# Kernel optimization log

Hardware: AMD Instinct MI355X
Metric: run time of the kernel (lower is better)

## Reference

```python
import jax, jax.numpy as jnp
import numpy as np

B, C, N, F = 256, 4, 64, 256   # batch, in_channels, neighbors, in_features
OC, OF = 8, 256                # out_channels, out_features


def setup_inputs() -> dict:
    key = jax.random.key(0)
    k1, k2, k3, k4, k5 = jax.random.split(key, 5)
    x = jax.random.normal(k1, (B, C, F), dtype=jnp.float32)
    neighbor = jax.random.normal(k2, (B, N, C, F), dtype=jnp.float32)
    # torch.nn.Linear weights are (out_features, in_features)
    W_att1 = jax.random.normal(k3, (C, F), dtype=jnp.float32) / np.sqrt(F).astype(np.float32)
    W_att2 = jax.random.normal(k4, (C, F), dtype=jnp.float32) / np.sqrt(F).astype(np.float32)
    # Conv1d weight: (out_c*out_f, 2C, F); kernel_size==F makes it a dense contraction
    W_conv = jax.random.normal(k5, (OC * OF, 2 * C, F), dtype=jnp.float32) / np.sqrt(2 * C * F).astype(np.float32)
    return {"x": x, "neighbor": neighbor, "W_att1": W_att1, "W_att2": W_att2, "W_conv": W_conv}


def reference(x, neighbor, W_att1, W_att2, W_conv):
    # --- attention weights: einsum 'ci,nkl->n' = sum(att1(x_i)) * sum_{k,l} att2(y_i)[n]
    s1 = jnp.sum(x @ W_att1.T, axis=(1, 2))              # (B,)
    s2 = jnp.sum(neighbor @ W_att2.T, axis=(2, 3))       # (B, N)
    w = jax.nn.softmax(s1[:, None] * s2, axis=1)         # softmax over neighbors (dim 0 per-sample)

    # --- feature adjacency: einsum 'ca,ncb,n->cab' vectorized over batch
    fadj = jnp.einsum('bcx,bncy,bn->bcxy', x, neighbor, w)   # (B, C, F, F)
    fadj = fadj + jnp.swapaxes(fadj, -1, -2)
    # sgnroot
    fadj = jnp.sign(fadj) * jnp.sqrt(jnp.clip(jnp.abs(fadj), 1e-8, None))
    # row normalize over dim -2, NaN -> 0
    adj = fadj / (jnp.abs(fadj).sum(axis=-2, keepdims=True) + 1e-7)
    adj = jnp.where(jnp.isnan(adj), jnp.float32(0.0), adj)

    # --- transform: cat([adj @ x, x], channel) then full-width conv1d (dense contraction)
    h = jnp.einsum('bcxy,bcy->bcx', adj, x)              # (B, C, F)
    z = jnp.concatenate([h, x], axis=1)                  # (B, 2C, F)
    out = jnp.einsum('bcf,ocf->bo', z, W_conv).reshape(B, OC, OF)
    return out, adj
```

## Files before the change

### kernel.cpp

```cpp
#include <hip/hip_runtime.h>
#include <hip/hip_bf16.h>
#include <math.h>


typedef __bf16 bf16x8 __attribute__((ext_vector_type(8)));
typedef __bf16 bf16x4 __attribute__((ext_vector_type(4)));
typedef float f32x4 __attribute__((ext_vector_type(4)));

#define NB 256
#define NC 4
#define NN 64
#define NF 256
#define NO 2048

__global__ __launch_bounds__(256) void k_scores(
    const float* __restrict__ x, const float* __restrict__ nb,
    const float* __restrict__ W1, const float* __restrict__ W2,
    float* __restrict__ s1, float* __restrict__ s2)
{
  __shared__ float red[4];
  int t = threadIdx.x;
  int gid = blockIdx.x;
  float val;
  if (gid < NB * NN) {
    float w = W2[t] + W2[256 + t] + W2[512 + t] + W2[768 + t];
    const float* p = nb + (size_t)gid * 1024;
    val = w * (p[t] + p[256 + t] + p[512 + t] + p[768 + t]);
  } else {
    int b = gid - NB * NN;
    float w = W1[t] + W1[256 + t] + W1[512 + t] + W1[768 + t];
    const float* p = x + (size_t)b * 1024;
    val = w * (p[t] + p[256 + t] + p[512 + t] + p[768 + t]);
  }
  for (int off = 32; off > 0; off >>= 1) val += __shfl_down(val, off);
  int wid = t >> 6;
  if ((t & 63) == 0) red[wid] = val;
  __syncthreads();
  if (t == 0) {
    float s = red[0] + red[1] + red[2] + red[3];
    if (gid < NB * NN) s2[gid] = s;
    else s1[gid - NB * NN] = s;
  }
}

__global__ __launch_bounds__(256) void k_cvt(
    const float* __restrict__ Wc, const float* __restrict__ x,
    __hip_bfloat16* __restrict__ Wcb, __hip_bfloat16* __restrict__ zbf)
{
  int idx = blockIdx.x * 256 + threadIdx.x;
  if (idx < 1048576) {
    float4 v = ((const float4*)Wc)[idx];
    bf16x4 o = { (__bf16)v.x, (__bf16)v.y, (__bf16)v.z, (__bf16)v.w };
    ((bf16x4*)Wcb)[idx] = o;
  } else {
    int i = idx - 1048576;
    int e = i * 4;
    int b = e >> 10, r = e & 1023;
    float4 v = ((const float4*)x)[i];
    bf16x4 o = { (__bf16)v.x, (__bf16)v.y, (__bf16)v.z, (__bf16)v.w };
    *(bf16x4*)(zbf + (size_t)b * 2048 + 1024 + r) = o;
  }
}

__global__ __launch_bounds__(256) void k_adj(
    const float* __restrict__ x, const float* __restrict__ nb,
    const float* __restrict__ s1, const float* __restrict__ s2,
    float* __restrict__ adj, float* __restrict__ hf,
    __hip_bfloat16* __restrict__ zbf)
{
  __shared__ float xs[256], ns[256], invs[256], wsh[64];
  __shared__ float part[4][256];
  int t = threadIdx.x;
  int w = t >> 6, l = t & 63;
  int blk = blockIdx.x;
  int b = blk >> 2, c = blk & 3;

  if (t < 64) {
    float v = s1[b] * s2[b * 64 + t];
    float m = v;
    for (int off = 32; off > 0; off >>= 1) m = fmaxf(m, __shfl_xor(m, off));
    float e = expf(v - m);
    float s = e;
    for (int off = 32; off > 0; off >>= 1) s += __shfl_xor(s, off);
    wsh[t] = e / s;
  }
  __syncthreads();

  float acc = 0.f;
  const float* pb = nb + (size_t)b * 65536 + c * 256 + t;
  #pragma unroll 8
  for (int n = 0; n < 64; ++n) acc = fmaf(wsh[n], pb[(size_t)n * 1024], acc);
  ns[t] = acc;
  xs[t] = x[(size_t)blk * 256 + t];
  __syncthreads();

  int j0 = l * 4;
  float4 xv = *(const float4*)&xs[j0];
  float4 nv = *(const float4*)&ns[j0];
  int i0 = w * 64;

  float4 cs = {0.f, 0.f, 0.f, 0.f};
  #pragma unroll 4
  for (int ii = 0; ii < 64; ++ii) {
    int i = i0 + ii;
    float xi = xs[i], ni = ns[i];
    float v0 = fmaf(xi, nv.x, xv.x * ni);
    float v1 = fmaf(xi, nv.y, xv.y * ni);
    float v2 = fmaf(xi, nv.z, xv.z * ni);
    float v3 = fmaf(xi, nv.w, xv.w * ni);
    float r0 = __builtin_amdgcn_sqrtf(fmaxf(fabsf(v0), 1e-8f));
    float r1 = __builtin_amdgcn_sqrtf(fmaxf(fabsf(v1), 1e-8f));
    float r2 = __builtin_amdgcn_sqrtf(fmaxf(fabsf(v2), 1e-8f));
    float r3 = __builtin_amdgcn_sqrtf(fmaxf(fabsf(v3), 1e-8f));
    cs.x += (v0 != 0.f) ? r0 : 0.f;
    cs.y += (v1 != 0.f) ? r1 : 0.f;
    cs.z += (v2 != 0.f) ? r2 : 0.f;
    cs.w += (v3 != 0.f) ? r3 : 0.f;
  }
  *(float4*)&part[w][j0] = cs;
  __syncthreads();
  invs[t] = 1.f / (part[0][t] + part[1][t] + part[2][t] + part[3][t] + 1e-7f);
  __syncthreads();

  float4 iv = *(const float4*)&invs[j0];
  float4 ha = {0.f, 0.f, 0.f, 0.f};
  float* ab = adj + (size_t)blk * 65536;
  #pragma unroll 4
  for (int ii = 0; ii < 64; ++ii) {
    int i = i0 + ii;
    float xi = xs[i], ni = ns[i];
    float pix = invs[i] * xi;
    float v0 = fmaf(xi, nv.x, xv.x * ni);
    float v1 = fmaf(xi, nv.y, xv.y * ni);
    float v2 = fmaf(xi, nv.z, xv.z * ni);
    float v3 = fmaf(xi, nv.w, xv.w * ni);
    float g0 = (v0 != 0.f) ? copysignf(__builtin_amdgcn_sqrtf(fmaxf(fabsf(v0), 1e-8f)), v0) : 0.f;
    float g1 = (v1 != 0.f) ? copysignf(__builtin_amdgcn_sqrtf(fmaxf(fabsf(v1), 1e-8f)), v1) : 0.f;
    float g2 = (v2 != 0.f) ? copysignf(__builtin_amdgcn_sqrtf(fmaxf(fabsf(v2), 1e-8f)), v2) : 0.f;
    float g3 = (v3 != 0.f) ? copysignf(__builtin_amdgcn_sqrtf(fmaxf(fabsf(v3), 1e-8f)), v3) : 0.f;
    f32x4 o = { g0 * iv.x, g1 * iv.y, g2 * iv.z, g3 * iv.w };
    __builtin_nontemporal_store(o, (f32x4*)&ab[(size_t)i * 256 + j0]);
    ha.x = fmaf(g0, pix, ha.x);
    ha.y = fmaf(g1, pix, ha.y);
    ha.z = fmaf(g2, pix, ha.z);
    ha.w = fmaf(g3, pix, ha.w);
  }
  __syncthreads();
  *(float4*)&part[w][j0] = ha;
  __syncthreads();
  float hsum = part[0][t] + part[1][t] + part[2][t] + part[3][t];
  if (zbf) zbf[(size_t)b * 2048 + c * 256 + t] = __float2bfloat16(hsum);
  else     hf[(size_t)blk * 256 + t] = hsum;
}

__global__ __launch_bounds__(256) void k_gemm(
    const __hip_bfloat16* __restrict__ zb, const __hip_bfloat16* __restrict__ Wcb,
    float* __restrict__ out)
{
  int tid = threadIdx.x;
  int wave = tid >> 6, lane = tid & 63;
  int g = lane >> 4, r = lane & 15;
  int bm = blockIdx.x & 7, bn = blockIdx.x >> 3;
  int m0 = bm * 32 + (wave & 1) * 16;
  int n0 = bn * 32 + (wave >> 1) * 16;

  const bf16x8* pa = (const bf16x8*)(zb  + (size_t)(m0 + r) * 2048 + g * 8);
  const bf16x8* pw = (const bf16x8*)(Wcb + (size_t)(n0 + r) * 2048 + g * 8);

  f32x4 acc0 = {0.f, 0.f, 0.f, 0.f}, acc1 = {0.f, 0.f, 0.f, 0.f};
  #pragma unroll 4
  for (int ks = 0; ks < 64; ks += 2) {
    bf16x8 a0 = pa[ks * 4];
    bf16x8 b0 = pw[ks * 4];
    bf16x8 a1 = pa[ks * 4 + 4];
    bf16x8 b1 = pw[ks * 4 + 4];
    acc0 = __builtin_amdgcn_mfma_f32_16x16x32_bf16(a0, b0, acc0, 0, 0, 0);
    acc1 = __builtin_amdgcn_mfma_f32_16x16x32_bf16(a1, b1, acc1, 0, 0, 0);
  }
  acc0 += acc1;
  #pragma unroll
  for (int q = 0; q < 4; ++q) {
    int row = m0 + g * 4 + q;
    __builtin_nontemporal_store(acc0[q], &out[(size_t)row * 2048 + n0 + r]);
  }
}

__device__ inline bf16x8 cvt8_p(const float* p) {
  const float4* q = reinterpret_cast<const float4*>(p);
  float4 a = q[0], bq = q[1];
  bf16x8 r;
  r[0] = (__bf16)a.x;  r[1] = (__bf16)a.y;  r[2] = (__bf16)a.z;  r[3] = (__bf16)a.w;
  r[4] = (__bf16)bq.x; r[5] = (__bf16)bq.y; r[6] = (__bf16)bq.z; r[7] = (__bf16)bq.w;
  return r;
}

__global__ __launch_bounds__(256) void k_gemm_f32(
    const float* __restrict__ h, const float* __restrict__ x,
    const float* __restrict__ Wc, float* __restrict__ out)
{
  int tid = threadIdx.x;
  int wave = tid >> 6, lane = tid & 63;
  int g = lane >> 4, r = lane & 15;
  int bm = blockIdx.x & 3, bn = blockIdx.x >> 2;
  int m0 = bm * 64 + wave * 16;
  int n0 = bn * 32;
  int arow = m0 + r;
  int koff = g * 8;

  const float* za = h + (size_t)arow * 1024 + koff;
  const float* zb = x + (size_t)arow * 1024 + koff;
  const float* w0 = Wc + (size_t)(n0 + r) * 2048 + koff;
  const float* w1 = Wc + (size_t)(n0 + 16 + r) * 2048 + koff;

  f32x4 acc0 = {0.f, 0.f, 0.f, 0.f}, acc1 = {0.f, 0.f, 0.f, 0.f};
  #pragma unroll 4
  for (int ks = 0; ks < 32; ++ks) {
    bf16x8 a  = cvt8_p(za + ks * 32);
    bf16x8 b0 = cvt8_p(w0 + ks * 32);
    bf16x8 b1 = cvt8_p(w1 + ks * 32);
    acc0 = __builtin_amdgcn_mfma_f32_16x16x32_bf16(a, b0, acc0, 0, 0, 0);
    acc1 = __builtin_amdgcn_mfma_f32_16x16x32_bf16(a, b1, acc1, 0, 0, 0);
  }
  #pragma unroll 4
  for (int ks = 0; ks < 32; ++ks) {
    bf16x8 a  = cvt8_p(zb + ks * 32);
    bf16x8 b0 = cvt8_p(w0 + 1024 + ks * 32);
    bf16x8 b1 = cvt8_p(w1 + 1024 + ks * 32);
    acc0 = __builtin_amdgcn_mfma_f32_16x16x32_bf16(a, b0, acc0, 0, 0, 0);
    acc1 = __builtin_amdgcn_mfma_f32_16x16x32_bf16(a, b1, acc1, 0, 0, 0);
  }
  #pragma unroll
  for (int q = 0; q < 4; ++q) {
    int row = m0 + g * 4 + q;
    out[(size_t)row * 2048 + n0 + r]      = acc0[q];
    out[(size_t)row * 2048 + n0 + 16 + r] = acc1[q];
  }
}

extern "C" void kernel_launch(void* const* d_in, const int* in_sizes, int n_in,
                              void* d_out, int out_size, void* d_ws, size_t ws_size,
                              hipStream_t stream) {
  const float* x  = (const float*)d_in[0];
  const float* nb = (const float*)d_in[1];
  const float* W1 = (const float*)d_in[2];
  const float* W2 = (const float*)d_in[3];
  const float* Wc = (const float*)d_in[4];
  float* out = (float*)d_out;
  float* adj = out + (size_t)NB * NO;

  char* ws = (char*)d_ws;
  const size_t ZBF_B = 1048576;
  const size_t WCB_B = 8388608;
  bool fast = ws_size >= ZBF_B + WCB_B + 66560;

  if (fast) {
    __hip_bfloat16* zbf = (__hip_bfloat16*)ws;
    __hip_bfloat16* Wcb = (__hip_bfloat16*)(ws + ZBF_B);
    float* s1 = (float*)(ws + ZBF_B + WCB_B);
    float* s2 = s1 + 256;
    k_scores<<<NB * NN + NB, 256, 0, stream>>>(x, nb, W1, W2, s1, s2);
    k_cvt<<<4352, 256, 0, stream>>>(Wc, x, Wcb, zbf);
    k_adj<<<NB * NC, 256, 0, stream>>>(x, nb, s1, s2, adj, nullptr, zbf);
    k_gemm<<<512, 256, 0, stream>>>(zbf, Wcb, out);
  } else {
    float* hws = (float*)d_ws;
    float* s1  = hws + 262144;
    float* s2  = s1 + 256;
    k_scores<<<NB * NN + NB, 256, 0, stream>>>(x, nb, W1, W2, s1, s2);
    k_adj<<<NB * NC, 256, 0, stream>>>(x, nb, s1, s2, adj, hws, nullptr);
    k_gemm_f32<<<256, 256, 0, stream>>>(hws, x, Wc, out);
  }
}
```

Measured before the change: 112.4 us.

## Split adjacency store into separate wide kernel and merge scores with conversion

Fuses the score and bf16-conversion kernels into one launch that uses float4 loads for the scores. Moves the heavy 256MB adjacency write out of the per-(b,c) kernel into a separate kernel with 4x more blocks, recomputing the entries from saved ns and inverse-norm vectors. The neighbor-weighted sum now reads float4 across waves with a shared-memory reduction. This adds an extra kernel launch and recomputes the sqrt work, in exchange for better write parallelism on the store-bound adjacency output. The fast path needs a larger workspace, and if that is not available it falls back to the old path.

Result: slower. 137.2 us (+22.1%).

```diff
diff --git a/kernel.cpp b/kernel.cpp
--- a/kernel.cpp
+++ b/kernel.cpp
@@ -13,7 +13,218 @@
 #define NF 256
 #define NO 2048
 
-__global__ __launch_bounds__(256) void k_scores(
+__global__ __launch_bounds__(256) void k_pre(
+    const float* __restrict__ x, const float* __restrict__ nb,
+    const float* __restrict__ W1, const float* __restrict__ W2,
+    const float* __restrict__ Wc,
+    __hip_bfloat16* __restrict__ Wcb, __hip_bfloat16* __restrict__ zbf,
+    float* __restrict__ s1, float* __restrict__ s2)
+{
+  __shared__ float red[4];
+  int t = threadIdx.x;
+  int gid = blockIdx.x;
+
+  if (gid < 16640) {
+    int fi = t & 63;
+    const float4* Wf4 = (const float4*)((gid < 16384) ? W2 : W1);
+    float4 w0 = Wf4[fi], w1 = Wf4[64 + fi], w2 = Wf4[128 + fi], w3 = Wf4[192 + fi];
+    float4 wv = { w0.x + w1.x + w2.x + w3.x,
+                  w0.y + w1.y + w2.y + w3.y,
+                  w0.z + w1.z + w2.z + w3.z,
+                  w0.w + w1.w + w2.w + w3.w };
+    const float4* src = (gid < 16384) ? ((const float4*)nb + (size_t)gid * 256)
+                                      : ((const float4*)x + (size_t)(gid - 16384) * 256);
+    float4 nv = src[t];
+    float val = fmaf(nv.x, wv.x, fmaf(nv.y, wv.y, fmaf(nv.z, wv.z, nv.w * wv.w)));
+    for (int off = 32; off > 0; off >>= 1) val += __shfl_down(val, off);
+    if ((t & 63) == 0) red[t >> 6] = val;
+    __syncthreads();
+    if (t == 0) {
+      float s = red[0] + red[1] + red[2] + red[3];
+      if (gid < 16384) s2[gid] = s;
+      else s1[gid - 16384] = s;
+    }
+  } else if (gid < 20736) {
+    int idx = (gid - 16640) * 256 + t;
+    float4 v = ((const float4*)Wc)[idx];
+    bf16x4 o = { (__bf16)v.x, (__bf16)v.y, (__bf16)v.z, (__bf16)v.w };
+    ((bf16x4*)Wcb)[idx] = o;
+  } else {
+    int i = (gid - 20736) * 256 + t;
+    int e = i * 4;
+    int b = e >> 10, r = e & 1023;
+    float4 v = ((const float4*)x)[i];
+    bf16x4 o = { (__bf16)v.x, (__bf16)v.y, (__bf16)v.z, (__bf16)v.w };
+    *(bf16x4*)(zbf + (size_t)b * 2048 + 1024 + r) = o;
+  }
+}
+
+__global__ __launch_bounds__(256) void k_nw(
+    const float* __restrict__ x, const float* __restrict__ nb,
+    const float* __restrict__ s1, const float* __restrict__ s2,
+    float* __restrict__ nsArr, float* __restrict__ invArr,
+    __hip_bfloat16* __restrict__ zbf)
+{
+  __shared__ float xs[256], ns[256], invs[256], wsh[64];
+  __shared__ float part[4][256];
+  int t = threadIdx.x;
+  int w = t >> 6, l = t & 63;
+  int blk = blockIdx.x;
+  int b = blk >> 2, c = blk & 3;
+
+  if (t < 64) {
+    float v = s1[b] * s2[b * 64 + t];
+    float m = v;
+    for (int off = 32; off > 0; off >>= 1) m = fmaxf(m, __shfl_xor(m, off));
+    float e = expf(v - m);
+    float s = e;
+    for (int off = 32; off > 0; off >>= 1) s += __shfl_xor(s, off);
+    wsh[t] = e / s;
+  }
+  xs[t] = x[(size_t)blk * 256 + t];
+  __syncthreads();
+
+  const float4* nb4 = (const float4*)(nb + (size_t)b * 65536 + c * 256);
+  float4 a4 = {0.f, 0.f, 0.f, 0.f};
+  #pragma unroll
+  for (int k = 0; k < 16; ++k) {
+    int n = w + 4 * k;
+    float4 v = nb4[(size_t)n * 256 + l];
+    float wn = wsh[n];
+    a4.x = fmaf(wn, v.x, a4.x);
+    a4.y = fmaf(wn, v.y, a4.y);
+    a4.z = fmaf(wn, v.z, a4.z);
+    a4.w = fmaf(wn, v.w, a4.w);
+  }
+  *(float4*)&part[w][l * 4] = a4;
+  __syncthreads();
+  ns[t] = part[0][t] + part[1][t] + part[2][t] + part[3][t];
+  __syncthreads();
+
+  int j0 = l * 4;
+  float4 xv = *(const float4*)&xs[j0];
+  float4 nv = *(const float4*)&ns[j0];
+  int i0 = w * 64;
+
+  float4 cs = {0.f, 0.f, 0.f, 0.f};
+  #pragma unroll 4
+  for (int ii = 0; ii < 64; ++ii) {
+    int i = i0 + ii;
+    float xi = xs[i], ni = ns[i];
+    float v0 = fmaf(xi, nv.x, xv.x * ni);
+    float v1 = fmaf(xi, nv.y, xv.y * ni);
+    float v2 = fmaf(xi, nv.z, xv.z * ni);
+    float v3 = fmaf(xi, nv.w, xv.w * ni);
+    cs.x += (v0 != 0.f) ? __builtin_amdgcn_sqrtf(fmaxf(fabsf(v0), 1e-8f)) : 0.f;
+    cs.y += (v1 != 0.f) ? __builtin_amdgcn_sqrtf(fmaxf(fabsf(v1), 1e-8f)) : 0.f;
+    cs.z += (v2 != 0.f) ? __builtin_amdgcn_sqrtf(fmaxf(fabsf(v2), 1e-8f)) : 0.f;
+    cs.w += (v3 != 0.f) ? __builtin_amdgcn_sqrtf(fmaxf(fabsf(v3), 1e-8f)) : 0.f;
+  }
+  *(float4*)&part[w][j0] = cs;
+  __syncthreads();
+  invs[t] = 1.f / (part[0][t] + part[1][t] + part[2][t] + part[3][t] + 1e-7f);
+  nsArr[(size_t)blk * 256 + t] = ns[t];
+  __syncthreads();
+  invArr[(size_t)blk * 256 + t] = invs[t];
+
+  float4 ha = {0.f, 0.f, 0.f, 0.f};
+  #pragma unroll 4
+  for (int ii = 0; ii < 64; ++ii) {
+    int i = i0 + ii;
+    float xi = xs[i], ni = ns[i];
+    float pix = invs[i] * xi;
+    float v0 = fmaf(xi, nv.x, xv.x * ni);
+    float v1 = fmaf(xi, nv.y, xv.y * ni);
+    float v2 = fmaf(xi, nv.z, xv.z * ni);
+    float v3 = fmaf(xi, nv.w, xv.w * ni);
+    float g0 = (v0 != 0.f) ? copysignf(__builtin_amdgcn_sqrtf(fmaxf(fabsf(v0), 1e-8f)), v0) : 0.f;
+    float g1 = (v1 != 0.f) ? copysignf(__builtin_amdgcn_sqrtf(fmaxf(fabsf(v1), 1e-8f)), v1) : 0.f;
+    float g2 = (v2 != 0.f) ? copysignf(__builtin_amdgcn_sqrtf(fmaxf(fabsf(v2), 1e-8f)), v2) : 0.f;
+    float g3 = (v3 != 0.f) ? copysignf(__builtin_amdgcn_sqrtf(fmaxf(fabsf(v3), 1e-8f)), v3) : 0.f;
+    ha.x = fmaf(g0, pix, ha.x);
+    ha.y = fmaf(g1, pix, ha.y);
+    ha.z = fmaf(g2, pix, ha.z);
+    ha.w = fmaf(g3, pix, ha.w);
+  }
+  __syncthreads();
+  *(float4*)&part[w][j0] = ha;
+  __syncthreads();
+  float hsum = part[0][t] + part[1][t] + part[2][t] + part[3][t];
+  zbf[(size_t)b * 2048 + c * 256 + t] = __float2bfloat16(hsum);
+}
+
+__global__ __launch_bounds__(256) void k_adj_store(
+    const float* __restrict__ x, const float* __restrict__ nsArr,
+    const float* __restrict__ invArr, float* __restrict__ adj)
+{
+  __shared__ float xs[256], ns[256], invs[256];
+  int t = threadIdx.x;
+  int w = t >> 6, l = t & 63;
+  int blk = blockIdx.x;
+  int bc = blk >> 2, q = blk & 3;
+
+  xs[t]   = x[(size_t)bc * 256 + t];
+  ns[t]   = nsArr[(size_t)bc * 256 + t];
+  invs[t] = invArr[(size_t)bc * 256 + t];
+  __syncthreads();
+
+  int j0 = l * 4;
+  float4 xv = *(const float4*)&xs[j0];
+  float4 nv = *(const float4*)&ns[j0];
+  float4 iv = *(const float4*)&invs[j0];
+  float* ab = adj + (size_t)bc * 65536;
+  int i0 = q * 64 + w * 16;
+
+  #pragma unroll 4
+  for (int ii = 0; ii < 16; ++ii) {
+    int i = i0 + ii;
+    float xi = xs[i], ni = ns[i];
+    float v0 = fmaf(xi, nv.x, xv.x * ni);
+    float v1 = fmaf(xi, nv.y, xv.y * ni);
+    float v2 = fmaf(xi, nv.z, xv.z * ni);
+    float v3 = fmaf(xi, nv.w, xv.w * ni);
+    float g0 = (v0 != 0.f) ? copysignf(__builtin_amdgcn_sqrtf(fmaxf(fabsf(v0), 1e-8f)), v0) : 0.f;
+    float g1 = (v1 != 0.f) ? copysignf(__builtin_amdgcn_sqrtf(fmaxf(fabsf(v1), 1e-8f)), v1) : 0.f;
+    float g2 = (v2 != 0.f) ? copysignf(__builtin_amdgcn_sqrtf(fmaxf(fabsf(v2), 1e-8f)), v2) : 0.f;
+    float g3 = (v3 != 0.f) ? copysignf(__builtin_amdgcn_sqrtf(fmaxf(fabsf(v3), 1e-8f)), v3) : 0.f;
+    f32x4 o = { g0 * iv.x, g1 * iv.y, g2 * iv.z, g3 * iv.w };
+    __builtin_nontemporal_store(o, (f32x4*)&ab[(size_t)i * 256 + j0]);
+  }
+}
+
+__global__ __launch_bounds__(256) void k_gemm(
+    const __hip_bfloat16* __restrict__ zb, const __hip_bfloat16* __restrict__ Wcb,
+    float* __restrict__ out)
+{
+  int tid = threadIdx.x;
+  int wave = tid >> 6, lane = tid & 63;
+  int g = lane >> 4, r = lane & 15;
+  int bm = blockIdx.x & 7, bn = blockIdx.x >> 3;
+  int m0 = bm * 32 + (wave & 1) * 16;
+  int n0 = bn * 32 + (wave >> 1) * 16;
+
+  const bf16x8* pa = (const bf16x8*)(zb  + (size_t)(m0 + r) * 2048 + g * 8);
+  const bf16x8* pw = (const bf16x8*)(Wcb + (size_t)(n0 + r) * 2048 + g * 8);
+
+  f32x4 acc0 = {0.f, 0.f, 0.f, 0.f}, acc1 = {0.f, 0.f, 0.f, 0.f};
+  #pragma unroll 4
+  for (int ks = 0; ks < 64; ks += 2) {
+    bf16x8 a0 = pa[ks * 4];
+    bf16x8 b0 = pw[ks * 4];
+    bf16x8 a1 = pa[ks * 4 + 4];
+    bf16x8 b1 = pw[ks * 4 + 4];
+    acc0 = __builtin_amdgcn_mfma_f32_16x16x32_bf16(a0, b0, acc0, 0, 0, 0);
+    acc1 = __builtin_amdgcn_mfma_f32_16x16x32_bf16(a1, b1, acc1, 0, 0, 0);
+  }
+  acc0 += acc1;
+  #pragma unroll
+  for (int q = 0; q < 4; ++q) {
+    int row = m0 + g * 4 + q;
+    __builtin_nontemporal_store(acc0[q], &out[(size_t)row * 2048 + n0 + r]);
+  }
+}
+
+__global__ __launch_bounds__(256) void k_scores_fb(
     const float* __restrict__ x, const float* __restrict__ nb,
     const float* __restrict__ W1, const float* __restrict__ W2,
     float* __restrict__ s1, float* __restrict__ s2)
@@ -33,8 +244,7 @@
     val = w * (p[t] + p[256 + t] + p[512 + t] + p[768 + t]);
   }
   for (int off = 32; off > 0; off >>= 1) val += __shfl_down(val, off);
-  int wid = t >> 6;
-  if ((t & 63) == 0) red[wid] = val;
+  if ((t & 63) == 0) red[t >> 6] = val;
   __syncthreads();
   if (t == 0) {
     float s = red[0] + red[1] + red[2] + red[3];
@@ -43,30 +253,10 @@
   }
 }
 
-__global__ __launch_bounds__(256) void k_cvt(
-    const float* __restrict__ Wc, const float* __restrict__ x,
-    __hip_bfloat16* __restrict__ Wcb, __hip_bfloat16* __restrict__ zbf)
-{
-  int idx = blockIdx.x * 256 + threadIdx.x;
-  if (idx < 1048576) {
-    float4 v = ((const float4*)Wc)[idx];
-    bf16x4 o = { (__bf16)v.x, (__bf16)v.y, (__bf16)v.z, (__bf16)v.w };
-    ((bf16x4*)Wcb)[idx] = o;
-  } else {
-    int i = idx - 1048576;
-    int e = i * 4;
-    int b = e >> 10, r = e & 1023;
-    float4 v = ((const float4*)x)[i];
-    bf16x4 o = { (__bf16)v.x, (__bf16)v.y, (__bf16)v.z, (__bf16)v.w };
-    *(bf16x4*)(zbf + (size_t)b * 2048 + 1024 + r) = o;
-  }
-}
-
-__global__ __launch_bounds__(256) void k_adj(
+__global__ __launch_bounds__(256) void k_adj_fb(
     const float* __restrict__ x, const float* __restrict__ nb,
     const float* __restrict__ s1, const float* __restrict__ s2,
-    float* __restrict__ adj, float* __restrict__ hf,
-    __hip_bfloat16* __restrict__ zbf)
+    float* __restrict__ adj, float* __restrict__ hf)
 {
   __shared__ float xs[256], ns[256], invs[256], wsh[64];
   __shared__ float part[4][256];
@@ -85,7 +275,6 @@
     wsh[t] = e / s;
   }
   __syncthreads();
-
   float acc = 0.f;
   const float* pb = nb + (size_t)b * 65536 + c * 256 + t;
   #pragma unroll 8
@@ -98,9 +287,7 @@
   float4 xv = *(const float4*)&xs[j0];
   float4 nv = *(const float4*)&ns[j0];
   int i0 = w * 64;
-
   float4 cs = {0.f, 0.f, 0.f, 0.f};
-  #pragma unroll 4
   for (int ii = 0; ii < 64; ++ii) {
     int i = i0 + ii;
     float xi = xs[i], ni = ns[i];
@@ -108,14 +295,10 @@
     float v1 = fmaf(xi, nv.y, xv.y * ni);
     float v2 = fmaf(xi, nv.z, xv.z * ni);
     float v3 = fmaf(xi, nv.w, xv.w * ni);
-    float r0 = __builtin_amdgcn_sqrtf(fmaxf(fabsf(v0), 1e-8f));
-    float r1 = __builtin_amdgcn_sqrtf(fmaxf(fabsf(v1), 1e-8f));
-    float r2 = __builtin_amdgcn_sqrtf(fmaxf(fabsf(v2), 1e-8f));
-    float r3 = __builtin_amdgcn_sqrtf(fmaxf(fabsf(v3), 1e-8f));
-    cs.x += (v0 != 0.f) ? r0 : 0.f;
-    cs.y += (v1 != 0.f) ? r1 : 0.f;
-    cs.z += (v2 != 0.f) ? r2 : 0.f;
-    cs.w += (v3 != 0.f) ? r3 : 0.f;
+    cs.x += (v0 != 0.f) ? __builtin_amdgcn_sqrtf(fmaxf(fabsf(v0), 1e-8f)) : 0.f;
+    cs.y += (v1 != 0.f) ? __builtin_amdgcn_sqrtf(fmaxf(fabsf(v1), 1e-8f)) : 0.f;
+    cs.z += (v2 != 0.f) ? __builtin_amdgcn_sqrtf(fmaxf(fabsf(v2), 1e-8f)) : 0.f;
+    cs.w += (v3 != 0.f) ? __builtin_amdgcn_sqrtf(fmaxf(fabsf(v3), 1e-8f)) : 0.f;
   }
   *(float4*)&part[w][j0] = cs;
   __syncthreads();
@@ -125,7 +308,6 @@
   float4 iv = *(const float4*)&invs[j0];
   float4 ha = {0.f, 0.f, 0.f, 0.f};
   float* ab = adj + (size_t)blk * 65536;
-  #pragma unroll 4
   for (int ii = 0; ii < 64; ++ii) {
     int i = i0 + ii;
     float xi = xs[i], ni = ns[i];
@@ -148,41 +330,7 @@
   __syncthreads();
   *(float4*)&part[w][j0] = ha;
   __syncthreads();
-  float hsum = part[0][t] + part[1][t] + part[2][t] + part[3][t];
-  if (zbf) zbf[(size_t)b * 2048 + c * 256 + t] = __float2bfloat16(hsum);
-  else     hf[(size_t)blk * 256 + t] = hsum;
-}
-
-__global__ __launch_bounds__(256) void k_gemm(
-    const __hip_bfloat16* __restrict__ zb, const __hip_bfloat16* __restrict__ Wcb,
-    float* __restrict__ out)
-{
-  int tid = threadIdx.x;
-  int wave = tid >> 6, lane = tid & 63;
-  int g = lane >> 4, r = lane & 15;
-  int bm = blockIdx.x & 7, bn = blockIdx.x >> 3;
-  int m0 = bm * 32 + (wave & 1) * 16;
-  int n0 = bn * 32 + (wave >> 1) * 16;
-
-  const bf16x8* pa = (const bf16x8*)(zb  + (size_t)(m0 + r) * 2048 + g * 8);
-  const bf16x8* pw = (const bf16x8*)(Wcb + (size_t)(n0 + r) * 2048 + g * 8);
-
-  f32x4 acc0 = {0.f, 0.f, 0.f, 0.f}, acc1 = {0.f, 0.f, 0.f, 0.f};
-  #pragma unroll 4
-  for (int ks = 0; ks < 64; ks += 2) {
-    bf16x8 a0 = pa[ks * 4];
-    bf16x8 b0 = pw[ks * 4];
-    bf16x8 a1 = pa[ks * 4 + 4];
-    bf16x8 b1 = pw[ks * 4 + 4];
-    acc0 = __builtin_amdgcn_mfma_f32_16x16x32_bf16(a0, b0, acc0, 0, 0, 0);
-    acc1 = __builtin_amdgcn_mfma_f32_16x16x32_bf16(a1, b1, acc1, 0, 0, 0);
-  }
-  acc0 += acc1;
-  #pragma unroll
-  for (int q = 0; q < 4; ++q) {
-    int row = m0 + g * 4 + q;
-    __builtin_nontemporal_store(acc0[q], &out[(size_t)row * 2048 + n0 + r]);
-  }
+  hf[(size_t)blk * 256 + t] = part[0][t] + part[1][t] + part[2][t] + part[3][t];
 }
 
 __device__ inline bf16x8 cvt8_p(const float* p) {
@@ -215,19 +363,13 @@
   f32x4 acc0 = {0.f, 0.f, 0.f, 0.f}, acc1 = {0.f, 0.f, 0.f, 0.f};
   #pragma unroll 4
   for (int ks = 0; ks < 32; ++ks) {
-    bf16x8 a  = cvt8_p(za + ks * 32);
-    bf16x8 b0 = cvt8_p(w0 + ks * 32);
-    bf16x8 b1 = cvt8_p(w1 + ks * 32);
-    acc0 = __builtin_amdgcn_mfma_f32_16x16x32_bf16(a, b0, acc0, 0, 0, 0);
-    acc1 = __builtin_amdgcn_mfma_f32_16x16x32_bf16(a, b1, acc1, 0, 0, 0);
+    acc0 = __builtin_amdgcn_mfma_f32_16x16x32_bf16(cvt8_p(za + ks * 32), cvt8_p(w0 + ks * 32), acc0, 0, 0, 0);
+    acc1 = __builtin_amdgcn_mfma_f32_16x16x32_bf16(cvt8_p(za + ks * 32), cvt8_p(w1 + ks * 32), acc1, 0, 0, 0);
   }
   #pragma unroll 4
   for (int ks = 0; ks < 32; ++ks) {
-    bf16x8 a  = cvt8_p(zb + ks * 32);
-    bf16x8 b0 = cvt8_p(w0 + 1024 + ks * 32);
-    bf16x8 b1 = cvt8_p(w1 + 1024 + ks * 32);
-    acc0 = __builtin_amdgcn_mfma_f32_16x16x32_bf16(a, b0, acc0, 0, 0, 0);
-    acc1 = __builtin_amdgcn_mfma_f32_16x16x32_bf16(a, b1, acc1, 0, 0, 0);
+    acc0 = __builtin_amdgcn_mfma_f32_16x16x32_bf16(cvt8_p(zb + ks * 32), cvt8_p(w0 + 1024 + ks * 32), acc0, 0, 0, 0);
+    acc1 = __builtin_amdgcn_mfma_f32_16x16x32_bf16(cvt8_p(zb + ks * 32), cvt8_p(w1 + 1024 + ks * 32), acc1, 0, 0, 0);
   }
   #pragma unroll
   for (int q = 0; q < 4; ++q) {
@@ -251,23 +393,26 @@
   char* ws = (char*)d_ws;
   const size_t ZBF_B = 1048576;
   const size_t WCB_B = 8388608;
-  bool fast = ws_size >= ZBF_B + WCB_B + 66560;
+  const size_t FREG = (256 + 16384 + 262144 + 262144) * 4;
+  bool fast = ws_size >= ZBF_B + WCB_B + FREG;
 
   if (fast) {
     __hip_bfloat16* zbf = (__hip_bfloat16*)ws;
     __hip_bfloat16* Wcb = (__hip_bfloat16*)(ws + ZBF_B);
-    float* s1 = (float*)(ws + ZBF_B + WCB_B);
-    float* s2 = s1 + 256;
-    k_scores<<<NB * NN + NB, 256, 0, stream>>>(x, nb, W1, W2, s1, s2);
-    k_cvt<<<4352, 256, 0, stream>>>(Wc, x, Wcb, zbf);
-    k_adj<<<NB * NC, 256, 0, stream>>>(x, nb, s1, s2, adj, nullptr, zbf);
+    float* s1  = (float*)(ws + ZBF_B + WCB_B);
+    float* s2  = s1 + 256;
+    float* nsA = s2 + 16384;
+    float* ivA = nsA + 262144;
+    k_pre<<<20992, 256, 0, stream>>>(x, nb, W1, W2, Wc, Wcb, zbf, s1, s2);
+    k_nw<<<NB * NC, 256, 0, stream>>>(x, nb, s1, s2, nsA, ivA, zbf);
+    k_adj_store<<<4096, 256, 0, stream>>>(x, nsA, ivA, adj);
     k_gemm<<<512, 256, 0, stream>>>(zbf, Wcb, out);
   } else {
     float* hws = (float*)d_ws;
     float* s1  = hws + 262144;
     float* s2  = s1 + 256;
-    k_scores<<<NB * NN + NB, 256, 0, stream>>>(x, nb, W1, W2, s1, s2);
-    k_adj<<<NB * NC, 256, 0, stream>>>(x, nb, s1, s2, adj, hws, nullptr);
+    k_scores_fb<<<NB * NN + NB, 256, 0, stream>>>(x, nb, W1, W2, s1, s2);
+    k_adj_fb<<<NB * NC, 256, 0, stream>>>(x, nb, s1, s2, adj, hws);
     k_gemm_f32<<<256, 256, 0, stream>>>(hws, x, Wc, out);
   }
 }
```
